# Performance work log

Measured on AMD Instinct MI355X. Metric: run time of the kernel, lower is better.

Reference implementation:

```python
import jax, jax.numpy as jnp
import numpy as np

B, L, D = 32, 512, 1024

def setup_inputs() -> dict:
    key = jax.random.key(0)
    ks = jax.random.split(key, 9)
    s = 0.02
    return {
        "query": jax.random.normal(ks[0], (B, L, D), jnp.float32),
        "context": jax.random.normal(ks[1], (B, L, D), jnp.float32),
        "W_in": jax.random.normal(ks[2], (D, D), jnp.float32) * s,
        "b_in": jax.random.normal(ks[3], (D,), jnp.float32) * s,
        "W_in2": jax.random.normal(ks[4], (D, D), jnp.float32) * s,
        "b_in2": jax.random.normal(ks[5], (D,), jnp.float32) * s,
        "W_out": jax.random.normal(ks[6], (L, D), jnp.float32) * s,  # windows_lens == L
        "W_fc": jax.random.normal(ks[7], (D, 2 * D), jnp.float32) * s,
        "b_fc": jax.random.normal(ks[8], (D,), jnp.float32) * s,
    }

def reference(query, context, W_in, b_in, W_in2, b_in2, W_out, W_fc, b_fc):
    # additive (Bahdanau) score: tanh(Wq q + Wc c) @ W_out^T -> [B, L, L]
    q = jnp.einsum('bld,ed->ble', query, W_in) + b_in
    c = jnp.einsum('bld,ed->ble', context, W_in2) + b_in2
    alpha = jnp.einsum('bld,wd->blw', jnp.tanh(q + c), W_out)  # [B, L, L]
    alpha = jax.nn.softmax(alpha, axis=-1)
    mix = jnp.einsum('blw,bwd->bld', alpha, context)           # bmm
    cat = jnp.concatenate([mix, context], axis=-1)             # [B, L, 2D]
    out = jnp.einsum('blf,df->bld', cat, W_fc) + b_fc
    return out, alpha
```

## Files before the change

### kernel.cpp

```cpp
#include <hip/hip_runtime.h>
#include <hip/hip_bf16.h>
#include <cstdint>

typedef unsigned short u16;
typedef unsigned int u32;
typedef __bf16 bf16x8 __attribute__((ext_vector_type(8)));
typedef float f32x4 __attribute__((ext_vector_type(4)));
typedef u16 u16x8 __attribute__((ext_vector_type(8)));

#define DEVINL __device__ __forceinline__

typedef __attribute__((address_space(1))) const u32 gbl_u32;
typedef __attribute__((address_space(3))) u32 lds_u32;

DEVINL void llds16(const void* g, void* l) {
  __builtin_amdgcn_global_load_lds((gbl_u32*)g, (lds_u32*)l, 16, 0, 0);
}

DEVINL u16 f2bf(float f) {
  union { float f; u32 i; } x; x.f = f;
  u32 r = x.i + 0x7FFFu + ((x.i >> 16) & 1u);
  return (u16)(r >> 16);
}

DEVINL float fast_tanh(float x) {
  x = fminf(10.f, fmaxf(-10.f, x));
  float e = __expf(2.f * x);
  return (e - 1.f) / (e + 1.f);
}

DEVINL bf16x8 cvt8(const float4& a, const float4& b) {
  bf16x8 r;
  r[0] = (__bf16)a.x; r[1] = (__bf16)a.y; r[2] = (__bf16)a.z; r[3] = (__bf16)a.w;
  r[4] = (__bf16)b.x; r[5] = (__bf16)b.y; r[6] = (__bf16)b.z; r[7] = (__bf16)b.w;
  return r;
}

DEVINL void tile64_one(const float* src, int srcld, int koff, u16* dst, int id) {
  int n = id >> 7, k8 = id & 127;
  int kb = k8 >> 3, h = k8 & 7;
  int u = h * 256 + ((n & 255) ^ (h << 1));
  const float* s = src + (size_t)n * srcld + koff + k8 * 8;
  *(bf16x8*)(dst + ((size_t)((n >> 8) * 16 + kb) * 2048 + u) * 8) =
      cvt8(*(const float4*)s, *(const float4*)(s + 4));
}

__global__ __launch_bounds__(256) void prep_weights(
    const float* __restrict__ W_in, const float* __restrict__ W_in2,
    const float* __restrict__ W_out, const float* __restrict__ W_fc,
    u16* __restrict__ wibf, u16* __restrict__ wi2bf, u16* __restrict__ wobf,
    u16* __restrict__ wf0, u16* __restrict__ wf1) {
  int id = blockIdx.x * 256 + threadIdx.x;
  if (id < 131072) {
    tile64_one(W_in, 1024, 0, wibf, id);
  } else if (id < 262144) {
    tile64_one(W_in2, 1024, 0, wi2bf, id - 131072);
  } else if (id < 327680) {
    int lid = id - 262144;
    int n = lid >> 7, k8 = lid & 127;
    int kb = k8 >> 2, h = k8 & 3;
    int u = h * 128 + ((n & 127) ^ (h << 1));
    const float* s = W_out + (size_t)n * 1024 + k8 * 8;
    *(bf16x8*)(wobf + ((size_t)((n >> 7) * 32 + kb) * 512 + u) * 8) =
        cvt8(*(const float4*)s, *(const float4*)(s + 4));
  } else if (id < 458752) {
    tile64_one(W_fc, 2048, 0, wf0, id - 327680);
  } else if (id < 589824) {
    tile64_one(W_fc, 2048, 1024, wf1, id - 458752);
  }
}

__global__ __launch_bounds__(256) void cvt_acts(const float* __restrict__ ctx,
                                                const float* __restrict__ query,
                                                u16* __restrict__ cbf,
                                                u16* __restrict__ qbf) {
  int i = blockIdx.x * 256 + threadIdx.x;
  const float* s;
  u16* d;
  if (i < 2097152) {
    s = ctx + (size_t)i * 8;
    d = cbf + (size_t)i * 8;
  } else {
    int j = i - 2097152;
    s = query + (size_t)j * 8;
    d = qbf + (size_t)j * 8;
  }
  *(bf16x8*)d = cvt8(*(const float4*)s, *(const float4*)(s + 4));
}

template <int NSEG, bool OUT_BF16, bool TANH>
__global__ __launch_bounds__(512) void gemm_nt10(
    const u16* __restrict__ A0, const u16* __restrict__ A1,
    const u16* __restrict__ Bt0, const u16* __restrict__ Bt1,
    const float* __restrict__ bias0, const float* __restrict__ bias1,
    void* __restrict__ Cout, int ldc) {
  __shared__ u16 As[3][16384];
  __shared__ u16 Bs[2][16384];
  const int tid = threadIdx.x, lane = tid & 63, w = tid >> 6;
  const int wr = w >> 2, wc = w & 3;

  const int NX = gridDim.x;
  const int total = NX * gridDim.y;
  const int flat = blockIdx.y * NX + blockIdx.x;
  const int wid = (flat & 7) * (total >> 3) + (flat >> 3);
  const int nb = wid % NX;
  const int n0 = nb * 256, m0 = (wid / NX) * 256;

  f32x4 acc[8][4];
#pragma unroll
  for (int i = 0; i < 8; ++i)
#pragma unroll
    for (int j = 0; j < 4; ++j) acc[i][j] = (f32x4)0.f;

  u32 asrc[4], bofs[4];
#pragma unroll
  for (int r = 0; r < 4; ++r) {
    int u = r * 512 + w * 64 + lane;
    int row = u >> 3, oct = (u & 7) ^ (row & 7);
    asrc[r] = (u32)(m0 + row) * 1024u + (u32)(oct * 8);
    bofs[r] = (u32)u * 8u;
  }

  const int NT = NSEG * 16;

  auto stageA = [&](int t) {
    const int seg = (NSEG == 2 && t >= 16) ? 1 : 0;
    const int kb = t - (seg << 4);
    const u16* Ap = seg ? A1 : A0;
    const u32 k0 = (u32)(kb << 6);
    u16* dst = As[t % 3];
#pragma unroll
    for (int q = 0; q < 4; ++q)
      llds16(Ap + (size_t)(asrc[q] + k0), dst + (q * 512 + w * 64) * 8);
  };
  auto stageA2 = [&](int t, int rp) {
    const int seg = (NSEG == 2 && t >= 16) ? 1 : 0;
    const int kb = t - (seg << 4);
    const u16* Ap = seg ? A1 : A0;
    const u32 k0 = (u32)(kb << 6);
    u16* dst = As[t % 3];
#pragma unroll
    for (int r = 0; r < 2; ++r) {
      const int q = rp * 2 + r;
      llds16(Ap + (size_t)(asrc[q] + k0), dst + (q * 512 + w * 64) * 8);
    }
  };
  auto stageB = [&](int t) {
    const int seg = (NSEG == 2 && t >= 16) ? 1 : 0;
    const int kb = t - (seg << 4);
    const u16* Bt = (seg ? Bt1 : Bt0) + ((size_t)(nb * 16 + kb) << 14);
    u16* dst = Bs[t & 1];
#pragma unroll
    for (int q = 0; q < 4; ++q)
      llds16(Bt + (size_t)bofs[q], dst + (q * 512 + w * 64) * 8);
  };
  auto stageB2 = [&](int t, int rp) {
    const int seg = (NSEG == 2 && t >= 16) ? 1 : 0;
    const int kb = t - (seg << 4);
    const u16* Bt = (seg ? Bt1 : Bt0) + ((size_t)(nb * 16 + kb) << 14);
    u16* dst = Bs[t & 1];
#pragma unroll
    for (int r = 0; r < 2; ++r) {
      const int q = rp * 2 + r;
      llds16(Bt + (size_t)bofs[q], dst + (q * 512 + w * 64) * 8);
    }
  };

  stageA(0);
  stageB(0);
  if (NT > 1) stageA(1);
  asm volatile("s_waitcnt vmcnt(6)" ::: "memory");
  __builtin_amdgcn_s_barrier();

  const int rl = lane & 15;
  for (int t = 0; t < NT; ++t) {
    const int ab = t % 3, bb = t & 1;
    const bool preB = (t + 1 < NT);
    const bool preA = (t + 2 < NT);
    bf16x8 af[8];

    {
      const int h = lane >> 4;
      const int jA = h ^ (rl & 7);
#pragma unroll
      for (int i = 0; i < 8; ++i)
        af[i] = *(const bf16x8*)&As[ab][((wr * 128 + i * 16 + rl) * 8 + jA) * 8];
      bf16x8 b0 = *(const bf16x8*)&Bs[bb][(h * 256 + ((wc * 64 + 0 + rl) ^ (h << 1))) * 8];
      bf16x8 b1 = *(const bf16x8*)&Bs[bb][(h * 256 + ((wc * 64 + 16 + rl) ^ (h << 1))) * 8];
      if (preB) stageB2(t + 1, 0);
      __builtin_amdgcn_s_barrier();
      asm volatile("s_waitcnt lgkmcnt(0)" ::: "memory");
      __builtin_amdgcn_sched_barrier(0);
      __builtin_amdgcn_s_setprio(1);
#pragma unroll
      for (int i = 0; i < 8; ++i) {
        acc[i][0] = __builtin_amdgcn_mfma_f32_16x16x32_bf16(af[i], b0, acc[i][0], 0, 0, 0);
        acc[i][1] = __builtin_amdgcn_mfma_f32_16x16x32_bf16(af[i], b1, acc[i][1], 0, 0, 0);
      }
      __builtin_amdgcn_s_setprio(0);
    }
    {
      const int h = lane >> 4;
      bf16x8 b2 = *(const bf16x8*)&Bs[bb][(h * 256 + ((wc * 64 + 32 + rl) ^ (h << 1))) * 8];
      bf16x8 b3 = *(const bf16x8*)&Bs[bb][(h * 256 + ((wc * 64 + 48 + rl) ^ (h << 1))) * 8];
      if (preB) stageB2(t + 1, 1);
      if (preB) asm volatile("s_waitcnt vmcnt(8)" ::: "memory");
      else      asm volatile("s_waitcnt vmcnt(0)" ::: "memory");
      __builtin_amdgcn_s_barrier();
      asm volatile("s_waitcnt lgkmcnt(0)" ::: "memory");
      __builtin_amdgcn_sched_barrier(0);
      __builtin_amdgcn_s_setprio(1);
#pragma unroll
      for (int i = 0; i < 8; ++i) {
        acc[i][2] = __builtin_amdgcn_mfma_f32_16x16x32_bf16(af[i], b2, acc[i][2], 0, 0, 0);
        acc[i][3] = __builtin_amdgcn_mfma_f32_16x16x32_bf16(af[i], b3, acc[i][3], 0, 0, 0);
      }
      __builtin_amdgcn_s_setprio(0);
    }
    {
      const int h = 4 + (lane >> 4);
      const int jA = h ^ (rl & 7);
#pragma unroll
      for (int i = 0; i < 8; ++i)
        af[i] = *(const bf16x8*)&As[ab][((wr * 128 + i * 16 + rl) * 8 + jA) * 8];
      bf16x8 b0 = *(const bf16x8*)&Bs[bb][(h * 256 + ((wc * 64 + 0 + rl) ^ (h << 1))) * 8];
      bf16x8 b1 = *(const bf16x8*)&Bs[bb][(h * 256 + ((wc * 64 + 16 + rl) ^ (h << 1))) * 8];
      if (preA) stageA2(t + 2, 0);
      __builtin_amdgcn_s_barrier();
      asm volatile("s_waitcnt lgkmcnt(0)" ::: "memory");
      __builtin_amdgcn_sched_barrier(0);
      __builtin_amdgcn_s_setprio(1);
#pragma unroll
      for (int i = 0; i < 8; ++i) {
        acc[i][0] = __builtin_amdgcn_mfma_f32_16x16x32_bf16(af[i], b0, acc[i][0], 0, 0, 0);
        acc[i][1] = __builtin_amdgcn_mfma_f32_16x16x32_bf16(af[i], b1, acc[i][1], 0, 0, 0);
      }
      __builtin_amdgcn_s_setprio(0);
    }
    {
      const int h = 4 + (lane >> 4);
      bf16x8 b2 = *(const bf16x8*)&Bs[bb][(h * 256 + ((wc * 64 + 32 + rl) ^ (h << 1))) * 8];
      bf16x8 b3 = *(const bf16x8*)&Bs[bb][(h * 256 + ((wc * 64 + 48 + rl) ^ (h << 1))) * 8];
      if (preA) stageA2(t + 2, 1);
      if (t < NT - 2)       asm volatile("s_waitcnt vmcnt(6)" ::: "memory");
      else if (t == NT - 2) asm volatile("s_waitcnt vmcnt(2)" ::: "memory");
      else                  asm volatile("s_waitcnt vmcnt(0)" ::: "memory");
      __builtin_amdgcn_s_barrier();
      asm volatile("s_waitcnt lgkmcnt(0)" ::: "memory");
      __builtin_amdgcn_sched_barrier(0);
      __builtin_amdgcn_s_setprio(1);
#pragma unroll
      for (int i = 0; i < 8; ++i) {
        acc[i][2] = __builtin_amdgcn_mfma_f32_16x16x32_bf16(af[i], b2, acc[i][2], 0, 0, 0);
        acc[i][3] = __builtin_amdgcn_mfma_f32_16x16x32_bf16(af[i], b3, acc[i][3], 0, 0, 0);
      }
      __builtin_amdgcn_s_setprio(0);
    }
  }

  const int rq = lane >> 4;
#pragma unroll
  for (int j = 0; j < 4; ++j) {
    const int gc = n0 + wc * 64 + j * 16 + rl;
    float bia = 0.f;
    if (bias0) bia += bias0[gc];
    if (NSEG == 2 && bias1) bia += bias1[gc];
#pragma unroll
    for (int i = 0; i < 8; ++i) {
#pragma unroll
      for (int r = 0; r < 4; ++r) {
        const int grow = m0 + wr * 128 + i * 16 + rq * 4 + r;
        float v = acc[i][j][r] + bia;
        if (TANH) v = fast_tanh(v);
        if (OUT_BF16)
          ((u16*)Cout)[(size_t)grow * ldc + gc] = f2bf(v);
        else
          ((float*)Cout)[(size_t)grow * ldc + gc] = v;
      }
    }
  }
}

__global__ __launch_bounds__(256) void score_softmax(
    const u16* __restrict__ A, const u16* __restrict__ Bt,
    float* __restrict__ alpha) {
  __shared__ u16 As[2][2048];
  __shared__ u16 Bs[2][16384];
  const int tid = threadIdx.x, lane = tid & 63, w = tid >> 6;
  const int m0 = blockIdx.x * 64;
  const int rl = lane & 15, rq = lane >> 4;

  f32x4 acc[32];
#pragma unroll
  for (int j = 0; j < 32; ++j) acc[j] = (f32x4)0.f;

  const int arow = tid >> 2;
  const u32 asrc = (u32)(m0 + arow) * 1024u + (u32)(((tid & 3) ^ (arow & 3)) * 8);

  auto stage = [&](int kb, int buf) {
    llds16(A + (size_t)(asrc + (u32)(kb << 5)), &As[buf][tid * 8]);
#pragma unroll
    for (int p = 0; p < 8; ++p) {
      int u = p * 256 + tid;
      int s = u >> 9;
      llds16(Bt + ((size_t)((s * 32 + kb) * 512 + (u & 511))) * 8,
             &Bs[buf][(p * 256 + w * 64) * 8]);
    }
  };
  auto compute = [&](int buf) {
    const int h = rq;
    const int row = w * 16 + rl;
    bf16x8 af = *(const bf16x8*)&As[buf][(row * 4 + (h ^ (row & 3))) * 8];
#pragma unroll
    for (int j = 0; j < 32; ++j) {
      const int nl = 16 * (j & 7) + rl;
      const int s = j >> 3;
      bf16x8 bv = *(const bf16x8*)&Bs[buf][(s * 512 + h * 128 + (nl ^ (h << 1))) * 8];
      acc[j] = __builtin_amdgcn_mfma_f32_16x16x32_bf16(af, bv, acc[j], 0, 0, 0);
    }
  };

  stage(0, 0);
  __syncthreads();
  for (int t = 0; t < 32; ++t) {
    const int c = t & 1;
    if (t + 1 < 32) stage(t + 1, c ^ 1);
    compute(c);
    __syncthreads();
  }

  float inv[4];
#pragma unroll
  for (int r = 0; r < 4; ++r) {
    float m = acc[0][r];
#pragma unroll
    for (int j = 1; j < 32; ++j) m = fmaxf(m, acc[j][r]);
#pragma unroll
    for (int mask = 1; mask < 16; mask <<= 1)
      m = fmaxf(m, __shfl_xor(m, mask, 64));
    float s = 0.f;
#pragma unroll
    for (int j = 0; j < 32; ++j) {
      acc[j][r] = __expf(acc[j][r] - m);
      s += acc[j][r];
    }
#pragma unroll
    for (int mask = 1; mask < 16; mask <<= 1) s += __shfl_xor(s, mask, 64);
    inv[r] = 1.f / s;
  }

  const int growb = m0 + w * 16 + rq * 4;
#pragma unroll
  for (int j = 0; j < 32; ++j) {
    const int gc = j * 16 + rl;
#pragma unroll
    for (int r = 0; r < 4; ++r)
      alpha[(size_t)(growb + r) * 512 + gc] = acc[j][r] * inv[r];
  }
}

__global__ __launch_bounds__(256) void gemm_nn3(
    const float* __restrict__ alpha, const u16* __restrict__ ctxb,
    u16* __restrict__ mix) {
  __shared__ u16 As[2][4096];
  __shared__ u16 Bs[2][4096];
  const int tid = threadIdx.x, lane = tid & 63, w = tid >> 6;
  const int wr = w >> 1, wc = w & 1;
  const int b = blockIdx.z;
  const int n0 = blockIdx.x * 128, m0 = blockIdx.y * 128;
  const int h = lane >> 4, rlx = (lane & 15) ^ (h << 1);
  const float* A = alpha + (size_t)b * 262144;
  u16* C = mix + (size_t)b * 524288;

  f32x4 acc[4][4];
#pragma unroll
  for (int i = 0; i < 4; ++i)
#pragma unroll
    for (int j = 0; j < 4; ++j) acc[i][j] = (f32x4)0.f;

  const int row0 = tid >> 2, cb = tid & 3, row1 = 64 + row0;
  const int unit0 = cb * 128 + (row0 ^ (cb << 1));
  const int unit1 = cb * 128 + (row1 ^ (cb << 1));
  const int kl = tid & 31, ng = tid >> 5;
  const int hb = kl >> 3, kp = kl & 7;

  float4 fr[4];
  u16x8 ub[2];

  auto stage = [&](int t) {
    const int k0 = t << 5;
    const float* p0 = A + (size_t)(m0 + row0) * 512 + k0 + cb * 8;
    const float* p1 = A + (size_t)(m0 + row1) * 512 + k0 + cb * 8;
    fr[0] = *(const float4*)p0; fr[1] = *(const float4*)(p0 + 4);
    fr[2] = *(const float4*)p1; fr[3] = *(const float4*)(p1 + 4);
    const u16* Cb = ctxb + (size_t)b * 524288 + (size_t)(k0 + kl) * 1024 +
                    n0 + ng * 16;
    ub[0] = *(const u16x8*)Cb; ub[1] = *(const u16x8*)(Cb + 8);
  };
  auto stage_fin = [&](int buf) {
    *(bf16x8*)&As[buf][unit0 * 8] = cvt8(fr[0], fr[1]);
    *(bf16x8*)&As[buf][unit1 * 8] = cvt8(fr[2], fr[3]);
#pragma unroll
    for (int j = 0; j < 16; ++j) {
      int n = ng * 16 + j;
      Bs[buf][(hb * 128 + (n ^ (hb << 1))) * 8 + kp] =
          (j < 8) ? ub[0][j] : ub[1][j - 8];
    }
  };
  auto compute = [&](int buf) {
    bf16x8 af[4], bfv[4];
#pragma unroll
    for (int i = 0; i < 4; ++i)
      af[i] = *(const bf16x8*)&As[buf][(h * 128 + wr * 64 + i * 16 + rlx) * 8];
#pragma unroll
    for (int j = 0; j < 4; ++j)
      bfv[j] = *(const bf16x8*)&Bs[buf][(h * 128 + wc * 64 + j * 16 + rlx) * 8];
#pragma unroll
    for (int i = 0; i < 4; ++i)
#pragma unroll
      for (int j = 0; j < 4; ++j)
        acc[i][j] =
            __builtin_amdgcn_mfma_f32_16x16x32_bf16(af[i], bfv[j], acc[i][j], 0, 0, 0);
  };

  stage(0);
  stage_fin(0);
  __syncthreads();
  for (int t = 0; t < 16; ++t) {
    const int cb_ = t & 1;
    if (t + 1 < 16) stage(t + 1);
    compute(cb_);
    if (t + 1 < 16) stage_fin(cb_ ^ 1);
    __syncthreads();
  }

  const int rl = lane & 15, rq = lane >> 4;
#pragma unroll
  for (int j = 0; j < 4; ++j) {
    const int gc = n0 + wc * 64 + j * 16 + rl;
#pragma unroll
    for (int i = 0; i < 4; ++i) {
#pragma unroll
      for (int r = 0; r < 4; ++r) {
        const int grow = m0 + wr * 64 + i * 16 + rq * 4 + r;
        C[(size_t)grow * 1024 + gc] = f2bf(acc[i][j][r]);
      }
    }
  }
}

extern "C" void kernel_launch(void* const* d_in, const int* in_sizes, int n_in,
                              void* d_out, int out_size, void* d_ws, size_t ws_size,
                              hipStream_t stream) {
  const float* query = (const float*)d_in[0];
  const float* ctx   = (const float*)d_in[1];
  const float* W_in  = (const float*)d_in[2];
  const float* b_in  = (const float*)d_in[3];
  const float* W_in2 = (const float*)d_in[4];
  const float* b_in2 = (const float*)d_in[5];
  const float* W_out = (const float*)d_in[6];
  const float* W_fc  = (const float*)d_in[7];
  const float* b_fc  = (const float*)d_in[8];

  float* out   = (float*)d_out;
  float* alpha = (float*)d_out + 16777216;

  u16* wibf_t  = (u16*)d_ws;
  u16* wi2bf_t = wibf_t + 1048576;
  u16* wobf_t  = wibf_t + 2097152;
  u16* wf0_t   = wibf_t + 2621440;
  u16* wf1_t   = wibf_t + 3670016;
  u16* t_ws    = (u16*)((char*)d_ws + 9437184);
  u16* cbf     = (u16*)((char*)d_ws + 42991616);
  u16* qbf     = (u16*)((char*)d_ws + 76546048);

  dim3 blk(256, 1, 1);
  dim3 blk5(512, 1, 1);

  prep_weights<<<dim3(2304), blk, 0, stream>>>(W_in, W_in2, W_out, W_fc,
                                               wibf_t, wi2bf_t, wobf_t, wf0_t,
                                               wf1_t);
  cvt_acts<<<dim3(16384), blk, 0, stream>>>(ctx, query, cbf, qbf);

  gemm_nt10<2, true, true><<<dim3(4, 64), blk5, 0, stream>>>(
      qbf, cbf, wibf_t, wi2bf_t, b_in, b_in2, t_ws, 1024);

  score_softmax<<<dim3(256), blk, 0, stream>>>(t_ws, wobf_t, alpha);

  gemm_nn3<<<dim3(8, 4, 32), blk, 0, stream>>>(alpha, cbf, t_ws);

  gemm_nt10<2, false, false><<<dim3(4, 64), blk5, 0, stream>>>(
      t_ws, cbf, wf0_t, wf1_t, b_fc, nullptr, out, 1024);
}
```

Measured before the change: 285.4 us.

## Emit bf16 alpha copy from softmax and remap GEMM block order

The softmax kernel now also writes a bf16 copy of alpha into the reused query buffer. The mix GEMM reads that copy instead of re-reading fp32 alpha and converting it, which halves the A-operand traffic. The gemm_nt10 block-to-tile mapping is replaced by a hardcoded swizzle for a 4x64 grid, meant to change how blocks share tiles across XCDs. In exchange, softmax does an extra 8 MB of scattered 2-byte stores, and the new swizzle only works for this grid shape.

```diff
diff --git a/kernel.cpp b/kernel.cpp
--- a/kernel.cpp
+++ b/kernel.cpp
@@ -99,12 +99,10 @@
   const int tid = threadIdx.x, lane = tid & 63, w = tid >> 6;
   const int wr = w >> 2, wc = w & 3;
 
-  const int NX = gridDim.x;
-  const int total = NX * gridDim.y;
-  const int flat = blockIdx.y * NX + blockIdx.x;
-  const int wid = (flat & 7) * (total >> 3) + (flat >> 3);
-  const int nb = wid % NX;
-  const int n0 = nb * 256, m0 = (wid / NX) * 256;
+  const int flat = blockIdx.y * 4 + blockIdx.x;
+  const int nb = (flat & 6) >> 1;
+  const int mb = ((flat & 1) << 5) | (flat >> 3);
+  const int n0 = nb * 256, m0 = mb * 256;
 
   f32x4 acc[8][4];
 #pragma unroll
@@ -283,7 +281,7 @@
 
 __global__ __launch_bounds__(256) void score_softmax(
     const u16* __restrict__ A, const u16* __restrict__ Bt,
-    float* __restrict__ alpha) {
+    float* __restrict__ alpha, u16* __restrict__ albf) {
   __shared__ u16 As[2][2048];
   __shared__ u16 Bs[2][16384];
   const int tid = threadIdx.x, lane = tid & 63, w = tid >> 6;
@@ -354,13 +352,16 @@
   for (int j = 0; j < 32; ++j) {
     const int gc = j * 16 + rl;
 #pragma unroll
-    for (int r = 0; r < 4; ++r)
-      alpha[(size_t)(growb + r) * 512 + gc] = acc[j][r] * inv[r];
-  }
-}
-
-__global__ __launch_bounds__(256) void gemm_nn3(
-    const float* __restrict__ alpha, const u16* __restrict__ ctxb,
+    for (int r = 0; r < 4; ++r) {
+      float v = acc[j][r] * inv[r];
+      alpha[(size_t)(growb + r) * 512 + gc] = v;
+      albf[(size_t)(growb + r) * 512 + gc] = f2bf(v);
+    }
+  }
+}
+
+__global__ __launch_bounds__(256) void gemm_nn4(
+    const u16* __restrict__ albf, const u16* __restrict__ ctxb,
     u16* __restrict__ mix) {
   __shared__ u16 As[2][4096];
   __shared__ u16 Bs[2][4096];
@@ -369,7 +370,7 @@
   const int b = blockIdx.z;
   const int n0 = blockIdx.x * 128, m0 = blockIdx.y * 128;
   const int h = lane >> 4, rlx = (lane & 15) ^ (h << 1);
-  const float* A = alpha + (size_t)b * 262144;
+  const u16* A = albf + (size_t)b * 262144;
   u16* C = mix + (size_t)b * 524288;
 
   f32x4 acc[4][4];
@@ -384,22 +385,20 @@
   const int kl = tid & 31, ng = tid >> 5;
   const int hb = kl >> 3, kp = kl & 7;
 
-  float4 fr[4];
+  u16x8 ar[2];
   u16x8 ub[2];
 
   auto stage = [&](int t) {
     const int k0 = t << 5;
-    const float* p0 = A + (size_t)(m0 + row0) * 512 + k0 + cb * 8;
-    const float* p1 = A + (size_t)(m0 + row1) * 512 + k0 + cb * 8;
-    fr[0] = *(const float4*)p0; fr[1] = *(const float4*)(p0 + 4);
-    fr[2] = *(const float4*)p1; fr[3] = *(const float4*)(p1 + 4);
+    ar[0] = *(const u16x8*)(A + (size_t)(m0 + row0) * 512 + k0 + cb * 8);
+    ar[1] = *(const u16x8*)(A + (size_t)(m0 + row1) * 512 + k0 + cb * 8);
     const u16* Cb = ctxb + (size_t)b * 524288 + (size_t)(k0 + kl) * 1024 +
                     n0 + ng * 16;
     ub[0] = *(const u16x8*)Cb; ub[1] = *(const u16x8*)(Cb + 8);
   };
   auto stage_fin = [&](int buf) {
-    *(bf16x8*)&As[buf][unit0 * 8] = cvt8(fr[0], fr[1]);
-    *(bf16x8*)&As[buf][unit1 * 8] = cvt8(fr[2], fr[3]);
+    *(u16x8*)&As[buf][unit0 * 8] = ar[0];
+    *(u16x8*)&As[buf][unit1 * 8] = ar[1];
 #pragma unroll
     for (int j = 0; j < 16; ++j) {
       int n = ng * 16 + j;
@@ -473,6 +472,7 @@
   u16* t_ws    = (u16*)((char*)d_ws + 9437184);
   u16* cbf     = (u16*)((char*)d_ws + 42991616);
   u16* qbf     = (u16*)((char*)d_ws + 76546048);
+  u16* albf    = qbf;
 
   dim3 blk(256, 1, 1);
   dim3 blk5(512, 1, 1);
@@ -485,9 +485,9 @@
   gemm_nt10<2, true, true><<<dim3(4, 64), blk5, 0, stream>>>(
       qbf, cbf, wibf_t, wi2bf_t, b_in, b_in2, t_ws, 1024);
 
-  score_softmax<<<dim3(256), blk, 0, stream>>>(t_ws, wobf_t, alpha);
-
-  gemm_nn3<<<dim3(8, 4, 32), blk, 0, stream>>>(alpha, cbf, t_ws);
+  score_softmax<<<dim3(256), blk, 0, stream>>>(t_ws, wobf_t, alpha, albf);
+
+  gemm_nn4<<<dim3(8, 4, 32), blk, 0, stream>>>(albf, cbf, t_ws);
 
   gemm_nt10<2, false, false><<<dim3(4, 64), blk5, 0, stream>>>(
       t_ws, cbf, wf0_t, wf1_t, b_fc, nullptr, out, 1024);
```

Measured after the change: 291.6 us. 2.2% more time.
